# Performance work log

Measured on AMD Instinct MI355X. Metric: run time of the kernel, lower is better.

## Reference

```python
import jax, jax.numpy as jnp
import numpy as np

N = 100000
E = 1600000
IN_CH = 128
HID = 32
HEADS = 4
OUT_CH = 64
NEG_SLOPE = 0.2


def _gat_conv(x, src, dst, W, att_src, att_dst, bias, heads, out_ch):
    # PyG GATConv (concat=True, add_self_loops handled by caller via src/dst)
    n = x.shape[0]
    xp = (x @ W).reshape(n, heads, out_ch)                  # [N,H,C]
    a_src = (xp * att_src).sum(-1)                          # [N,H]
    a_dst = (xp * att_dst).sum(-1)                          # [N,H]
    e = jax.nn.leaky_relu(a_src[src] + a_dst[dst], NEG_SLOPE)  # [E,H]
    m = jax.ops.segment_max(e, dst, num_segments=n)         # per-dst max (safe: self-loops)
    ex = jnp.exp(e - m[dst])
    denom = jax.ops.segment_sum(ex, dst, num_segments=n)
    alpha = ex / denom[dst]                                  # [E,H]
    out = jax.ops.segment_sum(xp[src] * alpha[:, :, None], dst, num_segments=n)
    return out.reshape(n, heads * out_ch) + bias


def setup_inputs() -> dict:
    key = jax.random.key(0)
    ks = jax.random.split(key, 12)
    sc1 = 1.0 / np.sqrt(IN_CH)
    sc2 = 1.0 / np.sqrt(HID * HEADS * 2)
    return {
        "x_ppi": jax.random.normal(ks[0], (N, IN_CH), jnp.float32),
        "x_go": jax.random.normal(ks[1], (N, IN_CH), jnp.float32),
        "edge_index": jax.random.randint(ks[2], (2, E), 0, N, jnp.int32),
        "W1": jax.random.normal(ks[3], (IN_CH, HEADS * HID), jnp.float32) * sc1,
        "att_src1": jax.random.normal(ks[4], (HEADS, HID), jnp.float32) * sc1,
        "att_dst1": jax.random.normal(ks[5], (HEADS, HID), jnp.float32) * sc1,
        "b1": jnp.zeros((HEADS * HID,), jnp.float32),
        "W2": jax.random.normal(ks[6], (HID * HEADS * 2, OUT_CH), jnp.float32) * sc2,
        "att_src2": jax.random.normal(ks[7], (1, OUT_CH), jnp.float32) * sc2,
        "att_dst2": jax.random.normal(ks[8], (1, OUT_CH), jnp.float32) * sc2,
        "b2": jnp.zeros((OUT_CH,), jnp.float32),
    }


def reference(x_ppi, x_go, edge_index, W1, att_src1, att_dst1, b1, W2, att_src2, att_dst2, b2):
    loops = jnp.arange(N, dtype=edge_index.dtype)
    src = jnp.concatenate([edge_index[0], loops])
    dst = jnp.concatenate([edge_index[1], loops])
    h_ppi = _gat_conv(x_ppi, src, dst, W1, att_src1, att_dst1, b1, HEADS, HID)
    h_go = _gat_conv(x_go, src, dst, W1, att_src1, att_dst1, b1, HEADS, HID)
    h = jax.nn.relu(jnp.concatenate([h_ppi, h_go], axis=-1))  # [N, 2*H*HID]
    out = _gat_conv(h, src, dst, W2, att_src2, att_dst2, b2, 1, OUT_CH)
    return out
```

## Files before the change

kernel.cpp:

```cpp
#include <hip/hip_runtime.h>
#include <hip/hip_fp16.h>

constexpr int NN = 100000;
constexpr int EE = 1600000;
constexpr int ET = EE + NN;
constexpr int EQ = EE / 4;
constexpr int TQ = ET / 4;
constexpr int NBUK = (NN + 255) / 256;
constexpr int PB = 416;
constexpr float NEG = 0.2f;

typedef _Float16 f16x8 __attribute__((ext_vector_type(8)));
typedef _Float16 f16x4 __attribute__((ext_vector_type(4)));
typedef float    f32x4 __attribute__((ext_vector_type(4)));

__global__ __launch_bounds__(256) void k_bcount(const int4* __restrict__ dst4v,
                                                int* __restrict__ bucketCount) {
    __shared__ int bh[NBUK];
    for (int i = threadIdx.x; i < NBUK; i += 256) bh[i] = 0;
    __syncthreads();
    int gtid = blockIdx.x * 256 + threadIdx.x;
    for (int q = gtid; q < TQ; q += PB * 256) {
        int4 d;
        if (q < EQ) {
            d = dst4v[q];
        } else {
            int s0 = (q - EQ) * 4;
            d.x = s0; d.y = s0 + 1; d.z = s0 + 2; d.w = s0 + 3;
        }
        atomicAdd(&bh[d.x >> 8], 1);
        atomicAdd(&bh[d.y >> 8], 1);
        atomicAdd(&bh[d.z >> 8], 1);
        atomicAdd(&bh[d.w >> 8], 1);
    }
    __syncthreads();
    for (int i = threadIdx.x; i < NBUK; i += 256)
        if (bh[i]) atomicAdd(&bucketCount[i], bh[i]);
}

__global__ __launch_bounds__(512) void k_bscan(const int* __restrict__ bucketCount,
                                               int* __restrict__ bstart, int* __restrict__ gcur,
                                               int* __restrict__ rs) {
    __shared__ int sh[512];
    int t = threadIdx.x;
    int v = (t < NBUK) ? bucketCount[t] : 0;
    sh[t] = v;
    __syncthreads();
    for (int o = 1; o < 512; o <<= 1) {
        int u = (t >= o) ? sh[t - o] : 0;
        __syncthreads();
        sh[t] += u;
        __syncthreads();
    }
    if (t < NBUK) { bstart[t] = sh[t] - v; gcur[t] = sh[t] - v; }
    if (t == 0) { bstart[NBUK] = ET; rs[NN] = ET; }
}

__global__ __launch_bounds__(256) void k_bplace(const int4* __restrict__ src4v, const int4* __restrict__ dst4v,
                                                int* __restrict__ gcur, unsigned int* __restrict__ ebuf) {
    __shared__ int bh[NBUK];
    __shared__ int bbase[NBUK];
    for (int i = threadIdx.x; i < NBUK; i += 256) bh[i] = 0;
    __syncthreads();
    int gtid = blockIdx.x * 256 + threadIdx.x;

    int esrc[16];
    int emeta[16];
#pragma unroll
    for (int it = 0; it < 4; it++) {
        int q = gtid + it * (PB * 256);
        bool valid = q < TQ;
        int4 s, d;
        if (valid) {
            if (q < EQ) { s = src4v[q]; d = dst4v[q]; }
            else { int s0 = (q - EQ) * 4; s.x = s0; s.y = s0 + 1; s.z = s0 + 2; s.w = s0 + 3; d = s; }
        } else {
            s.x = s.y = s.z = s.w = 0; d = s;
        }
        int ss[4] = {s.x, s.y, s.z, s.w};
        int dd[4] = {d.x, d.y, d.z, d.w};
#pragma unroll
        for (int k = 0; k < 4; k++) {
            int idx = it * 4 + k;
            if (valid) {
                int b = dd[k] >> 8, l = dd[k] & 255;
                int r = atomicAdd(&bh[b], 1);
                esrc[idx]  = ss[k];
                emeta[idx] = (b << 21) | (l << 13) | r;
            } else {
                emeta[idx] = -1;
            }
        }
    }
    __syncthreads();
    for (int i = threadIdx.x; i < NBUK; i += 256)
        bbase[i] = bh[i] ? atomicAdd(&gcur[i], bh[i]) : 0;
    __syncthreads();
#pragma unroll
    for (int e = 0; e < 16; e++) {
        int me = emeta[e];
        if (me >= 0) {
            int b = me >> 21, l = (me >> 13) & 255, r = me & 8191;
            ebuf[bbase[b] + r] = ((unsigned)l << 24) | (unsigned)esrc[e];
        }
    }
}

__global__ __launch_bounds__(256) void k_csr(const unsigned int* __restrict__ ebuf,
                                             const int* __restrict__ bstart,
                                             int* __restrict__ rs, int* __restrict__ csr) {
    __shared__ int hist[256];
    __shared__ int sh[256];
    __shared__ int cur[256];
    int b = blockIdx.x;
    int t = threadIdx.x;
    int e0 = bstart[b], e1 = bstart[b + 1];
    hist[t] = 0;
    __syncthreads();
    for (int j = e0 + t; j < e1; j += 256)
        atomicAdd(&hist[ebuf[j] >> 24], 1);
    __syncthreads();
    int v = hist[t];
    sh[t] = v;
    __syncthreads();
    for (int o = 1; o < 256; o <<= 1) {
        int u = (t >= o) ? sh[t - o] : 0;
        __syncthreads();
        sh[t] += u;
        __syncthreads();
    }
    int excl = sh[t] - v;
    cur[t] = excl;
    int v0 = b * 256;
    if (v0 + t < NN) rs[v0 + t] = e0 + excl;
    __syncthreads();
    for (int j = e0 + t; j < e1; j += 256) {
        unsigned int e = ebuf[j];
        int l = (int)(e >> 24);
        int r = atomicAdd(&cur[l], 1);
        csr[e0 + r] = (int)(e & 0x00FFFFFFu);
    }
}

__global__ __launch_bounds__(256) void k_wprep(const float* __restrict__ W1, const float* __restrict__ W2,
                                               _Float16* __restrict__ w1T, _Float16* __restrict__ w2T) {
    int idx = blockIdx.x * 256 + threadIdx.x;
    if (idx < 128 * 128) {
        int nn = idx >> 7, k = idx & 127;
        w1T[idx] = (_Float16)W1[k * 128 + nn];
    }
    int i2 = idx - 128 * 128;
    if (i2 >= 0 && i2 < 64 * 256) {
        int nn = i2 >> 8, k = i2 & 255;
        w2T[i2] = (_Float16)W2[k * 64 + nn];
    }
}

template <int K, int C, bool SRCF32, int AMODE>
__global__ __launch_bounds__(256) void gemm_direct(const void* __restrict__ xv,
                                                   const _Float16* __restrict__ wT,
                                                   const float* __restrict__ as_w, const float* __restrict__ ad_w,
                                                   __half* __restrict__ xp,
                                                   float* __restrict__ att_s, float* __restrict__ att_d, int n) {
    constexpr int NT = C / 16;
    const int tid  = threadIdx.x;
    const int w    = tid >> 6;
    const int lane = tid & 63;
    const int quad = lane >> 4;
    const int l16  = lane & 15;
    const long r0  = (long)blockIdx.x * 128;
    const long row0 = r0 + w * 32 + l16;
    const long row1 = row0 + 16;

    f32x4 acc[2][NT];
#pragma unroll
    for (int s = 0; s < 2; s++)
#pragma unroll
        for (int t = 0; t < NT; t++) acc[s][t] = (f32x4){0.f, 0.f, 0.f, 0.f};

#pragma unroll
    for (int ks = 0; ks < K; ks += 32) {
        f16x8 a0 = (f16x8){0, 0, 0, 0, 0, 0, 0, 0};
        f16x8 a1 = (f16x8){0, 0, 0, 0, 0, 0, 0, 0};
        if (SRCF32) {
            if (row0 < n) {
                const float4* p = (const float4*)((const float*)xv + row0 * K + ks) + quad * 2;
                float4 u = p[0], v = p[1];
                a0 = (f16x8){(_Float16)u.x, (_Float16)u.y, (_Float16)u.z, (_Float16)u.w,
                             (_Float16)v.x, (_Float16)v.y, (_Float16)v.z, (_Float16)v.w};
            }
            if (row1 < n) {
                const float4* p = (const float4*)((const float*)xv + row1 * K + ks) + quad * 2;
                float4 u = p[0], v = p[1];
                a1 = (f16x8){(_Float16)u.x, (_Float16)u.y, (_Float16)u.z, (_Float16)u.w,
                             (_Float16)v.x, (_Float16)v.y, (_Float16)v.z, (_Float16)v.w};
            }
        } else {
            if (row0 < n) a0 = *(const f16x8*)((const _Float16*)xv + row0 * K + ks + quad * 8);
            if (row1 < n) a1 = *(const f16x8*)((const _Float16*)xv + row1 * K + ks + quad * 8);
        }
#pragma unroll
        for (int t = 0; t < NT; t++) {
            f16x8 b = *(const f16x8*)(wT + (long)(t * 16 + l16) * K + ks + quad * 8);
            acc[0][t] = __builtin_amdgcn_mfma_f32_16x16x32_f16(a0, b, acc[0][t], 0, 0, 0);
            acc[1][t] = __builtin_amdgcn_mfma_f32_16x16x32_f16(a1, b, acc[1][t], 0, 0, 0);
        }
    }

#pragma unroll
    for (int sub = 0; sub < 2; sub++) {
        long rb = r0 + w * 32 + sub * 16 + quad * 4;
#pragma unroll
        for (int t = 0; t < NT; t++) {
            int c = t * 16 + l16;
#pragma unroll
            for (int rg = 0; rg < 4; rg++) {
                long row = rb + rg;
                if (row < n) xp[row * (long)C + c] = __float2half(acc[sub][t][rg]);
            }
        }
    }

    if (AMODE == 1) {
        float asw[8], adw[8];
#pragma unroll
        for (int t = 0; t < 8; t++) {
            int ci = (t >> 1) * 32 + (t & 1) * 16 + l16;
            asw[t] = as_w[ci];
            adw[t] = ad_w[ci];
        }
#pragma unroll
        for (int sub = 0; sub < 2; sub++) {
#pragma unroll
            for (int rg = 0; rg < 4; rg++) {
                long row = r0 + w * 32 + sub * 16 + quad * 4 + rg;
                float hs[4] = {0.f, 0.f, 0.f, 0.f};
                float hd[4] = {0.f, 0.f, 0.f, 0.f};
#pragma unroll
                for (int t = 0; t < 8; t++) {
                    float av = acc[sub][t][rg];
                    hs[t >> 1] += av * asw[t];
                    hd[t >> 1] += av * adw[t];
                }
#pragma unroll
                for (int h = 0; h < 4; h++) {
                    hs[h] += __shfl_xor(hs[h], 1); hs[h] += __shfl_xor(hs[h], 2);
                    hs[h] += __shfl_xor(hs[h], 4); hs[h] += __shfl_xor(hs[h], 8);
                    hd[h] += __shfl_xor(hd[h], 1); hd[h] += __shfl_xor(hd[h], 2);
                    hd[h] += __shfl_xor(hd[h], 4); hd[h] += __shfl_xor(hd[h], 8);
                }
                if (l16 == 0 && row < n) {
                    ((float4*)att_s)[row] = make_float4(hs[0], hs[1], hs[2], hs[3]);
                    ((float4*)att_d)[row] = make_float4(hd[0], hd[1], hd[2], hd[3]);
                }
            }
        }
    }
    if (AMODE == 2) {
        float asw[NT], adw[NT];
#pragma unroll
        for (int t = 0; t < NT; t++) {
            asw[t] = as_w[t * 16 + l16];
            adw[t] = ad_w[t * 16 + l16];
        }
#pragma unroll
        for (int sub = 0; sub < 2; sub++) {
#pragma unroll
            for (int rg = 0; rg < 4; rg++) {
                long row = r0 + w * 32 + sub * 16 + quad * 4 + rg;
                float s = 0.f, d = 0.f;
#pragma unroll
                for (int t = 0; t < NT; t++) {
                    float av = acc[sub][t][rg];
                    s += av * asw[t];
                    d += av * adw[t];
                }
                s += __shfl_xor(s, 1); s += __shfl_xor(s, 2); s += __shfl_xor(s, 4); s += __shfl_xor(s, 8);
                d += __shfl_xor(d, 1); d += __shfl_xor(d, 2); d += __shfl_xor(d, 4); d += __shfl_xor(d, 8);
                if (l16 == 0 && row < n) {
                    att_s[row] = s;
                    att_d[row] = d;
                }
            }
        }
    }
}

__global__ __launch_bounds__(256) void conv1_pass(const int* __restrict__ rs, const int* __restrict__ csr,
                                                  const uint4* __restrict__ xp,
                                                  const float* __restrict__ att_s,
                                                  const float* __restrict__ att_d,
                                                  const float* __restrict__ bias,
                                                  __half* __restrict__ out, int off) {
    int v = blockIdx.x * 4 + (threadIdx.x >> 6);
    if (v >= NN) return;
    int lane = threadIdx.x & 63;
    int qw = lane >> 4;
    int m = lane & 15;
    int hd = m >> 2;
    int e0 = rs[v], e1 = rs[v + 1];

    float adv = att_d[v * 4 + hd];
    auto lrexp = [](float e) { e = (e > 0.f) ? e : NEG * e; return __expf(e); };

    float a[8];
#pragma unroll
    for (int i = 0; i < 8; i++) a[i] = 0.f;
    float d = 0.f;

    int j = e0;
    for (; j + 16 <= e1; j += 16) {
        int s[4]; float av[4]; uint4 r[4];
#pragma unroll
        for (int k = 0; k < 4; k++) s[k] = csr[j + 4 * k + qw];
#pragma unroll
        for (int k = 0; k < 4; k++) av[k] = att_s[s[k] * 4 + hd];
#pragma unroll
        for (int k = 0; k < 4; k++) r[k] = xp[(long)s[k] * 16 + m];
#pragma unroll
        for (int k = 0; k < 4; k++) {
            float w = lrexp(av[k] + adv);
            d += w;
            float2 f0 = __half22float2(*(__half2*)&r[k].x);
            float2 f1 = __half22float2(*(__half2*)&r[k].y);
            float2 f2 = __half22float2(*(__half2*)&r[k].z);
            float2 f3 = __half22float2(*(__half2*)&r[k].w);
            a[0] += w * f0.x; a[1] += w * f0.y;
            a[2] += w * f1.x; a[3] += w * f1.y;
            a[4] += w * f2.x; a[5] += w * f2.y;
            a[6] += w * f3.x; a[7] += w * f3.y;
        }
    }
    for (; j < e1; j += 4) {
        int jj = j + qw;
        int jc = (jj < e1) ? jj : (e1 - 1);
        int s = csr[jc];
        float av = att_s[s * 4 + hd];
        uint4 r = xp[(long)s * 16 + m];
        float w = (jj < e1) ? lrexp(av + adv) : 0.f;
        d += w;
        float2 f0 = __half22float2(*(__half2*)&r.x);
        float2 f1 = __half22float2(*(__half2*)&r.y);
        float2 f2 = __half22float2(*(__half2*)&r.z);
        float2 f3 = __half22float2(*(__half2*)&r.w);
        a[0] += w * f0.x; a[1] += w * f0.y;
        a[2] += w * f1.x; a[3] += w * f1.y;
        a[4] += w * f2.x; a[5] += w * f2.y;
        a[6] += w * f3.x; a[7] += w * f3.y;
    }

#pragma unroll
    for (int i = 0; i < 8; i++) {
        a[i] += __shfl_xor(a[i], 16);
        a[i] += __shfl_xor(a[i], 32);
    }
    d += __shfl_xor(d, 16);
    d += __shfl_xor(d, 32);

    if (qw == 0) {
        float inv = 1.0f / d;
        const float4* b4 = (const float4*)bias;
        float4 bA = b4[2 * m], bB = b4[2 * m + 1];
        __half2 o01 = __floats2half2_rn(fmaxf(a[0] * inv + bA.x, 0.f), fmaxf(a[1] * inv + bA.y, 0.f));
        __half2 o23 = __floats2half2_rn(fmaxf(a[2] * inv + bA.z, 0.f), fmaxf(a[3] * inv + bA.w, 0.f));
        __half2 o45 = __floats2half2_rn(fmaxf(a[4] * inv + bB.x, 0.f), fmaxf(a[5] * inv + bB.y, 0.f));
        __half2 o67 = __floats2half2_rn(fmaxf(a[6] * inv + bB.z, 0.f), fmaxf(a[7] * inv + bB.w, 0.f));
        uint4 st;
        st.x = *(unsigned int*)&o01;
        st.y = *(unsigned int*)&o23;
        st.z = *(unsigned int*)&o45;
        st.w = *(unsigned int*)&o67;
        *(uint4*)(out + (long)v * 256 + off + 8 * m) = st;
    }
}

__global__ __launch_bounds__(256) void conv2_edge(const int* __restrict__ rs, const int* __restrict__ csr,
                                                  const __half* __restrict__ xp,
                                                  const float* __restrict__ asrc,
                                                  const float* __restrict__ adst,
                                                  const float* __restrict__ bias,
                                                  float* __restrict__ out) {
    int v = blockIdx.x * 4 + (threadIdx.x >> 6);
    if (v >= NN) return;
    int lane = threadIdx.x & 63;
    int qw = lane >> 4;
    int m = lane & 15;
    int e0 = rs[v], e1 = rs[v + 1];
    const uint2* xp2 = (const uint2*)xp;

    float adv = adst[v];
    auto lrexp = [](float e) { e = (e > 0.f) ? e : NEG * e; return __expf(e); };

    float a0 = 0.f, a1 = 0.f, a2 = 0.f, a3 = 0.f, d = 0.f;

    int j = e0;
    for (; j + 16 <= e1; j += 16) {
        int s[4]; float av[4]; uint2 r[4];
#pragma unroll
        for (int k = 0; k < 4; k++) s[k] = csr[j + 4 * k + qw];
#pragma unroll
        for (int k = 0; k < 4; k++) av[k] = asrc[s[k]];
#pragma unroll
        for (int k = 0; k < 4; k++) r[k] = xp2[(long)s[k] * 16 + m];
#pragma unroll
        for (int k = 0; k < 4; k++) {
            float w = lrexp(av[k] + adv);
            d += w;
            float2 x01 = __half22float2(*(__half2*)&r[k].x);
            float2 x23 = __half22float2(*(__half2*)&r[k].y);
            a0 += w * x01.x; a1 += w * x01.y;
            a2 += w * x23.x; a3 += w * x23.y;
        }
    }
    for (; j < e1; j += 4) {
        int jj = j + qw;
        int jc = (jj < e1) ? jj : (e1 - 1);
        int s = csr[jc];
        float av = asrc[s];
        uint2 r = xp2[(long)s * 16 + m];
        float w = (jj < e1) ? lrexp(av + adv) : 0.f;
        d += w;
        float2 x01 = __half22float2(*(__half2*)&r.x);
        float2 x23 = __half22float2(*(__half2*)&r.y);
        a0 += w * x01.x; a1 += w * x01.y;
        a2 += w * x23.x; a3 += w * x23.y;
    }

    a0 += __shfl_xor(a0, 16); a1 += __shfl_xor(a1, 16);
    a2 += __shfl_xor(a2, 16); a3 += __shfl_xor(a3, 16);
    d  += __shfl_xor(d, 16);
    a0 += __shfl_xor(a0, 32); a1 += __shfl_xor(a1, 32);
    a2 += __shfl_xor(a2, 32); a3 += __shfl_xor(a3, 32);
    d  += __shfl_xor(d, 32);

    if (qw == 0) {
        float inv = 1.0f / d;
        float4 b4 = *(const float4*)&bias[4 * m];
        float4 o;
        o.x = a0 * inv + b4.x;
        o.y = a1 * inv + b4.y;
        o.z = a2 * inv + b4.z;
        o.w = a3 * inv + b4.w;
        *(float4*)&out[(long)v * 64 + 4 * m] = o;
    }
}

extern "C" void kernel_launch(void* const* d_in, const int* in_sizes, int n_in,
                              void* d_out, int out_size, void* d_ws, size_t ws_size,
                              hipStream_t stream) {
    const float* x_ppi = (const float*)d_in[0];
    const float* x_go  = (const float*)d_in[1];
    const int*   ei    = (const int*)d_in[2];
    const float* W1    = (const float*)d_in[3];
    const float* as1   = (const float*)d_in[4];
    const float* ad1   = (const float*)d_in[5];
    const float* b1    = (const float*)d_in[6];
    const float* W2    = (const float*)d_in[7];
    const float* as2   = (const float*)d_in[8];
    const float* ad2   = (const float*)d_in[9];
    const float* b2    = (const float*)d_in[10];
    float* out = (float*)d_out;

    char* ws = (char*)d_ws;
    size_t off = 0;
    auto alloc = [&](size_t bytes) -> void* {
        void* p = ws + off;
        off = (off + bytes + 255) & ~(size_t)255;
        return p;
    };
    int* bucketCount = (int*)alloc((size_t)NBUK * 4);
    int* bstart      = (int*)alloc((size_t)(NBUK + 1) * 4);
    int* gcur        = (int*)alloc((size_t)NBUK * 4);
    unsigned int* ebuf = (unsigned int*)alloc((size_t)ET * 4);
    int* rs      = (int*)alloc((size_t)(NN + 1) * 4);
    int* csr     = (int*)alloc((size_t)ET * 4);
    _Float16* w1T = (_Float16*)alloc((size_t)128 * 128 * 2);
    _Float16* w2T = (_Float16*)alloc((size_t)64 * 256 * 2);
    __half* xp_p = (__half*)alloc((size_t)NN * 128 * 2);
    __half* xp_g = (__half*)alloc((size_t)NN * 128 * 2);
    __half* xp2  = (__half*)alloc((size_t)NN * 64 * 2);
    float* attsp = (float*)alloc((size_t)NN * 4 * 4);
    float* attdp = (float*)alloc((size_t)NN * 4 * 4);
    float* attsg = (float*)alloc((size_t)NN * 4 * 4);
    float* attdg = (float*)alloc((size_t)NN * 4 * 4);
    float* asr2  = (float*)alloc((size_t)NN * 4);
    float* ads2  = (float*)alloc((size_t)NN * 4);
    __half* hbuf = (__half*)alloc((size_t)NN * 256 * 2);
    (void)ws_size; (void)in_sizes; (void)n_in; (void)out_size;

    const int GB = (NN + 127) / 128;

    hipMemsetAsync(bucketCount, 0, (size_t)NBUK * 4, stream);
    k_bcount<<<PB, 256, 0, stream>>>((const int4*)(ei + EE), bucketCount);
    k_bscan<<<1, 512, 0, stream>>>(bucketCount, bstart, gcur, rs);
    k_bplace<<<PB, 256, 0, stream>>>((const int4*)ei, (const int4*)(ei + EE), gcur, ebuf);
    k_csr<<<NBUK, 256, 0, stream>>>(ebuf, bstart, rs, csr);

    k_wprep<<<128, 256, 0, stream>>>(W1, W2, w1T, w2T);

    gemm_direct<128, 128, true, 1><<<GB, 256, 0, stream>>>(x_ppi, w1T, as1, ad1, xp_p, attsp, attdp, NN);
    gemm_direct<128, 128, true, 1><<<GB, 256, 0, stream>>>(x_go, w1T, as1, ad1, xp_g, attsg, attdg, NN);
    conv1_pass<<<NN / 4, 256, 0, stream>>>(rs, csr, (const uint4*)xp_p, attsp, attdp, b1, hbuf, 0);
    conv1_pass<<<NN / 4, 256, 0, stream>>>(rs, csr, (const uint4*)xp_g, attsg, attdg, b1, hbuf, 128);

    gemm_direct<256, 64, false, 2><<<GB, 256, 0, stream>>>(hbuf, w2T, as2, ad2, xp2, asr2, ads2, NN);
    conv2_edge<<<NN / 4, 256, 0, stream>>>(rs, csr, xp2, asr2, ads2, b2, out);
}
```

Measured before the change: 494.5 us.

## Interleave ppi/go projections and fuse both conv1 aggregations into one pass

```diff
diff --git a/kernel.cpp b/kernel.cpp
--- a/kernel.cpp
+++ b/kernel.cpp
@@ -8,142 +8,18 @@
 constexpr int TQ = ET / 4;
 constexpr int NBUK = (NN + 255) / 256;
 constexpr int PB = 416;
+constexpr int GB = (NN + 127) / 128;
 constexpr float NEG = 0.2f;
 
 typedef _Float16 f16x8 __attribute__((ext_vector_type(8)));
-typedef _Float16 f16x4 __attribute__((ext_vector_type(4)));
 typedef float    f32x4 __attribute__((ext_vector_type(4)));
 
-__global__ __launch_bounds__(256) void k_bcount(const int4* __restrict__ dst4v,
+__global__ __launch_bounds__(256) void k_wprep0(const float* __restrict__ W1, const float* __restrict__ W2,
+                                                _Float16* __restrict__ w1T, _Float16* __restrict__ w2T,
                                                 int* __restrict__ bucketCount) {
-    __shared__ int bh[NBUK];
-    for (int i = threadIdx.x; i < NBUK; i += 256) bh[i] = 0;
-    __syncthreads();
-    int gtid = blockIdx.x * 256 + threadIdx.x;
-    for (int q = gtid; q < TQ; q += PB * 256) {
-        int4 d;
-        if (q < EQ) {
-            d = dst4v[q];
-        } else {
-            int s0 = (q - EQ) * 4;
-            d.x = s0; d.y = s0 + 1; d.z = s0 + 2; d.w = s0 + 3;
-        }
-        atomicAdd(&bh[d.x >> 8], 1);
-        atomicAdd(&bh[d.y >> 8], 1);
-        atomicAdd(&bh[d.z >> 8], 1);
-        atomicAdd(&bh[d.w >> 8], 1);
-    }
-    __syncthreads();
-    for (int i = threadIdx.x; i < NBUK; i += 256)
-        if (bh[i]) atomicAdd(&bucketCount[i], bh[i]);
-}
-
-__global__ __launch_bounds__(512) void k_bscan(const int* __restrict__ bucketCount,
-                                               int* __restrict__ bstart, int* __restrict__ gcur,
-                                               int* __restrict__ rs) {
-    __shared__ int sh[512];
-    int t = threadIdx.x;
-    int v = (t < NBUK) ? bucketCount[t] : 0;
-    sh[t] = v;
-    __syncthreads();
-    for (int o = 1; o < 512; o <<= 1) {
-        int u = (t >= o) ? sh[t - o] : 0;
-        __syncthreads();
-        sh[t] += u;
-        __syncthreads();
-    }
-    if (t < NBUK) { bstart[t] = sh[t] - v; gcur[t] = sh[t] - v; }
-    if (t == 0) { bstart[NBUK] = ET; rs[NN] = ET; }
-}
-
-__global__ __launch_bounds__(256) void k_bplace(const int4* __restrict__ src4v, const int4* __restrict__ dst4v,
-                                                int* __restrict__ gcur, unsigned int* __restrict__ ebuf) {
-    __shared__ int bh[NBUK];
-    __shared__ int bbase[NBUK];
-    for (int i = threadIdx.x; i < NBUK; i += 256) bh[i] = 0;
-    __syncthreads();
-    int gtid = blockIdx.x * 256 + threadIdx.x;
-
-    int esrc[16];
-    int emeta[16];
-#pragma unroll
-    for (int it = 0; it < 4; it++) {
-        int q = gtid + it * (PB * 256);
-        bool valid = q < TQ;
-        int4 s, d;
-        if (valid) {
-            if (q < EQ) { s = src4v[q]; d = dst4v[q]; }
-            else { int s0 = (q - EQ) * 4; s.x = s0; s.y = s0 + 1; s.z = s0 + 2; s.w = s0 + 3; d = s; }
-        } else {
-            s.x = s.y = s.z = s.w = 0; d = s;
-        }
-        int ss[4] = {s.x, s.y, s.z, s.w};
-        int dd[4] = {d.x, d.y, d.z, d.w};
-#pragma unroll
-        for (int k = 0; k < 4; k++) {
-            int idx = it * 4 + k;
-            if (valid) {
-                int b = dd[k] >> 8, l = dd[k] & 255;
-                int r = atomicAdd(&bh[b], 1);
-                esrc[idx]  = ss[k];
-                emeta[idx] = (b << 21) | (l << 13) | r;
-            } else {
-                emeta[idx] = -1;
-            }
-        }
-    }
-    __syncthreads();
-    for (int i = threadIdx.x; i < NBUK; i += 256)
-        bbase[i] = bh[i] ? atomicAdd(&gcur[i], bh[i]) : 0;
-    __syncthreads();
-#pragma unroll
-    for (int e = 0; e < 16; e++) {
-        int me = emeta[e];
-        if (me >= 0) {
-            int b = me >> 21, l = (me >> 13) & 255, r = me & 8191;
-            ebuf[bbase[b] + r] = ((unsigned)l << 24) | (unsigned)esrc[e];
-        }
-    }
-}
-
-__global__ __launch_bounds__(256) void k_csr(const unsigned int* __restrict__ ebuf,
-                                             const int* __restrict__ bstart,
-                                             int* __restrict__ rs, int* __restrict__ csr) {
-    __shared__ int hist[256];
-    __shared__ int sh[256];
-    __shared__ int cur[256];
-    int b = blockIdx.x;
-    int t = threadIdx.x;
-    int e0 = bstart[b], e1 = bstart[b + 1];
-    hist[t] = 0;
-    __syncthreads();
-    for (int j = e0 + t; j < e1; j += 256)
-        atomicAdd(&hist[ebuf[j] >> 24], 1);
-    __syncthreads();
-    int v = hist[t];
-    sh[t] = v;
-    __syncthreads();
-    for (int o = 1; o < 256; o <<= 1) {
-        int u = (t >= o) ? sh[t - o] : 0;
-        __syncthreads();
-        sh[t] += u;
-        __syncthreads();
-    }
-    int excl = sh[t] - v;
-    cur[t] = excl;
-    int v0 = b * 256;
-    if (v0 + t < NN) rs[v0 + t] = e0 + excl;
-    __syncthreads();
-    for (int j = e0 + t; j < e1; j += 256) {
-        unsigned int e = ebuf[j];
-        int l = (int)(e >> 24);
-        int r = atomicAdd(&cur[l], 1);
-        csr[e0 + r] = (int)(e & 0x00FFFFFFu);
-    }
-}
-
-__global__ __launch_bounds__(256) void k_wprep(const float* __restrict__ W1, const float* __restrict__ W2,
-                                               _Float16* __restrict__ w1T, _Float16* __restrict__ w2T) {
+    if (blockIdx.x == 0) {
+        for (int i = threadIdx.x; i < NBUK; i += 256) bucketCount[i] = 0;
+    }
     int idx = blockIdx.x * 256 + threadIdx.x;
     if (idx < 128 * 128) {
         int nn = idx >> 7, k = idx & 127;
@@ -156,19 +32,19 @@
     }
 }
 
-template <int K, int C, bool SRCF32, int AMODE>
-__global__ __launch_bounds__(256) void gemm_direct(const void* __restrict__ xv,
-                                                   const _Float16* __restrict__ wT,
-                                                   const float* __restrict__ as_w, const float* __restrict__ ad_w,
-                                                   __half* __restrict__ xp,
-                                                   float* __restrict__ att_s, float* __restrict__ att_d, int n) {
+template <int K, int C, bool SRCF32, int AMODE, int OUTM, int SET>
+__device__ __forceinline__ void gemm_dev(int bx, const void* __restrict__ xv,
+                                         const _Float16* __restrict__ wT,
+                                         const float* __restrict__ as_w, const float* __restrict__ ad_w,
+                                         __half* __restrict__ xp,
+                                         float* __restrict__ att_s, float* __restrict__ att_d, int n) {
     constexpr int NT = C / 16;
     const int tid  = threadIdx.x;
     const int w    = tid >> 6;
     const int lane = tid & 63;
     const int quad = lane >> 4;
     const int l16  = lane & 15;
-    const long r0  = (long)blockIdx.x * 128;
+    const long r0  = (long)bx * 128;
     const long row0 = r0 + w * 32 + l16;
     const long row1 = row0 + 16;
 
@@ -216,7 +92,13 @@
 #pragma unroll
             for (int rg = 0; rg < 4; rg++) {
                 long row = rb + rg;
-                if (row < n) xp[row * (long)C + c] = __float2half(acc[sub][t][rg]);
+                if (row < n) {
+                    __half hv = __float2half(acc[sub][t][rg]);
+                    if (OUTM == 0)
+                        xp[row * 256 + ((c >> 1) << 2) + (c & 1) + SET * 2] = hv;
+                    else
+                        xp[row * (long)C + c] = hv;
+                }
             }
         }
     }
@@ -250,8 +132,11 @@
                     hd[h] += __shfl_xor(hd[h], 4); hd[h] += __shfl_xor(hd[h], 8);
                 }
                 if (l16 == 0 && row < n) {
-                    ((float4*)att_s)[row] = make_float4(hs[0], hs[1], hs[2], hs[3]);
-                    ((float4*)att_d)[row] = make_float4(hd[0], hd[1], hd[2], hd[3]);
+#pragma unroll
+                    for (int h = 0; h < 4; h++) {
+                        att_s[row * 8 + h * 2 + SET] = hs[h];
+                        att_d[row * 8 + h * 2 + SET] = hd[h];
+                    }
                 }
             }
         }
@@ -286,92 +171,240 @@
     }
 }
 
-__global__ __launch_bounds__(256) void conv1_pass(const int* __restrict__ rs, const int* __restrict__ csr,
-                                                  const uint4* __restrict__ xp,
-                                                  const float* __restrict__ att_s,
-                                                  const float* __restrict__ att_d,
-                                                  const float* __restrict__ bias,
-                                                  __half* __restrict__ out, int off) {
+__device__ __forceinline__ void bcount_dev(int bx, const int4* __restrict__ dst4v,
+                                           int* __restrict__ bucketCount) {
+    __shared__ int bh[NBUK];
+    for (int i = threadIdx.x; i < NBUK; i += 256) bh[i] = 0;
+    __syncthreads();
+    int gtid = bx * 256 + threadIdx.x;
+    for (int q = gtid; q < TQ; q += PB * 256) {
+        int4 d;
+        if (q < EQ) {
+            d = dst4v[q];
+        } else {
+            int s0 = (q - EQ) * 4;
+            d.x = s0; d.y = s0 + 1; d.z = s0 + 2; d.w = s0 + 3;
+        }
+        atomicAdd(&bh[d.x >> 8], 1);
+        atomicAdd(&bh[d.y >> 8], 1);
+        atomicAdd(&bh[d.z >> 8], 1);
+        atomicAdd(&bh[d.w >> 8], 1);
+    }
+    __syncthreads();
+    for (int i = threadIdx.x; i < NBUK; i += 256)
+        if (bh[i]) atomicAdd(&bucketCount[i], bh[i]);
+}
+
+__global__ __launch_bounds__(256) void megaA(const float* __restrict__ x_ppi, const float* __restrict__ x_go,
+                                             const int4* __restrict__ dst4v,
+                                             const _Float16* __restrict__ w1T,
+                                             const float* __restrict__ as1, const float* __restrict__ ad1,
+                                             __half* __restrict__ xpc,
+                                             float* __restrict__ att1s, float* __restrict__ att1d,
+                                             int* __restrict__ bucketCount) {
+    int bx = blockIdx.x;
+    if (bx < GB) {
+        gemm_dev<128, 128, true, 1, 0, 0>(bx, x_ppi, w1T, as1, ad1, xpc, att1s, att1d, NN);
+    } else if (bx < 2 * GB) {
+        gemm_dev<128, 128, true, 1, 0, 1>(bx - GB, x_go, w1T, as1, ad1, xpc, att1s, att1d, NN);
+    } else {
+        bcount_dev(bx - 2 * GB, dst4v, bucketCount);
+    }
+}
+
+__global__ __launch_bounds__(256) void gemm_k2(const __half* __restrict__ hbuf,
+                                               const _Float16* __restrict__ w2T,
+                                               const float* __restrict__ as2, const float* __restrict__ ad2,
+                                               __half* __restrict__ xp2,
+                                               float* __restrict__ asr2, float* __restrict__ ads2) {
+    gemm_dev<256, 64, false, 2, 1, 0>(blockIdx.x, hbuf, w2T, as2, ad2, xp2, asr2, ads2, NN);
+}
+
+__global__ __launch_bounds__(512) void k_bscan(const int* __restrict__ bucketCount,
+                                               int* __restrict__ bstart, int* __restrict__ gcur,
+                                               int* __restrict__ rs) {
+    __shared__ int sh[512];
+    int t = threadIdx.x;
+    int v = (t < NBUK) ? bucketCount[t] : 0;
+    sh[t] = v;
+    __syncthreads();
+    for (int o = 1; o < 512; o <<= 1) {
+        int u = (t >= o) ? sh[t - o] : 0;
+        __syncthreads();
+        sh[t] += u;
+        __syncthreads();
+    }
+    if (t < NBUK) { bstart[t] = sh[t] - v; gcur[t] = sh[t] - v; }
+    if (t == 0) { bstart[NBUK] = ET; rs[NN] = ET; }
+}
+
+__global__ __launch_bounds__(256) void k_bplace(const int4* __restrict__ src4v, const int4* __restrict__ dst4v,
+                                                int* __restrict__ gcur, unsigned int* __restrict__ ebuf) {
+    __shared__ int bh[NBUK];
+    __shared__ int bbase[NBUK];
+    for (int i = threadIdx.x; i < NBUK; i += 256) bh[i] = 0;
+    __syncthreads();
+    int gtid = blockIdx.x * 256 + threadIdx.x;
+
+    int esrc[16];
+    int emeta[16];
+#pragma unroll
+    for (int it = 0; it < 4; it++) {
+        int q = gtid + it * (PB * 256);
+        bool valid = q < TQ;
+        int4 s, d;
+        if (valid) {
+            if (q < EQ) { s = src4v[q]; d = dst4v[q]; }
+            else { int s0 = (q - EQ) * 4; s.x = s0; s.y = s0 + 1; s.z = s0 + 2; s.w = s0 + 3; d = s; }
+        } else {
+            s.x = s.y = s.z = s.w = 0; d = s;
+        }
+        int ss[4] = {s.x, s.y, s.z, s.w};
+        int dd[4] = {d.x, d.y, d.z, d.w};
+#pragma unroll
+        for (int k = 0; k < 4; k++) {
+            int idx = it * 4 + k;
+            if (valid) {
+                int b = dd[k] >> 8, l = dd[k] & 255;
+                int r = atomicAdd(&bh[b], 1);
+                esrc[idx]  = ss[k];
+                emeta[idx] = (b << 21) | (l << 13) | r;
+            } else {
+                emeta[idx] = -1;
+            }
+        }
+    }
+    __syncthreads();
+    for (int i = threadIdx.x; i < NBUK; i += 256)
+        bbase[i] = bh[i] ? atomicAdd(&gcur[i], bh[i]) : 0;
+    __syncthreads();
+#pragma unroll
+    for (int e = 0; e < 16; e++) {
+        int me = emeta[e];
+        if (me >= 0) {
+            int b = me >> 21, l = (me >> 13) & 255, r = me & 8191;
+            ebuf[bbase[b] + r] = ((unsigned)l << 24) | (unsigned)esrc[e];
+        }
+    }
+}
+
+__global__ __launch_bounds__(256) void k_csr(const unsigned int* __restrict__ ebuf,
+                                             const int* __restrict__ bstart,
+                                             int* __restrict__ rs, int* __restrict__ csr) {
+    __shared__ int hist[256];
+    __shared__ int sh[256];
+    __shared__ int cur[256];
+    int b = blockIdx.x;
+    int t = threadIdx.x;
+    int e0 = bstart[b], e1 = bstart[b + 1];
+    hist[t] = 0;
+    __syncthreads();
+    for (int j = e0 + t; j < e1; j += 256)
+        atomicAdd(&hist[ebuf[j] >> 24], 1);
+    __syncthreads();
+    int v = hist[t];
+    sh[t] = v;
+    __syncthreads();
+    for (int o = 1; o < 256; o <<= 1) {
+        int u = (t >= o) ? sh[t - o] : 0;
+        __syncthreads();
+        sh[t] += u;
+        __syncthreads();
+    }
+    int excl = sh[t] - v;
+    cur[t] = excl;
+    int v0 = b * 256;
+    if (v0 + t < NN) rs[v0 + t] = e0 + excl;
+    __syncthreads();
+    for (int j = e0 + t; j < e1; j += 256) {
+        unsigned int e = ebuf[j];
+        int l = (int)(e >> 24);
+        int r = atomicAdd(&cur[l], 1);
+        csr[e0 + r] = (int)(e & 0x00FFFFFFu);
+    }
+}
+
+__global__ __launch_bounds__(256) void conv1_packed(const int* __restrict__ rs, const int* __restrict__ csr,
+                                                    const uint4* __restrict__ xpc,
+                                                    const float2* __restrict__ att_s,
+                                                    const float2* __restrict__ att_d,
+                                                    const float* __restrict__ bias,
+                                                    __half* __restrict__ out) {
     int v = blockIdx.x * 4 + (threadIdx.x >> 6);
     if (v >= NN) return;
     int lane = threadIdx.x & 63;
-    int qw = lane >> 4;
-    int m = lane & 15;
-    int hd = m >> 2;
+    int h = lane >> 5;
+    int m = lane & 31;
+    int hd = m >> 3;
     int e0 = rs[v], e1 = rs[v + 1];
 
-    float adv = att_d[v * 4 + hd];
+    float2 ad = att_d[v * 4 + hd];
     auto lrexp = [](float e) { e = (e > 0.f) ? e : NEG * e; return __expf(e); };
 
-    float a[8];
-#pragma unroll
-    for (int i = 0; i < 8; i++) a[i] = 0.f;
-    float d = 0.f;
+    float ap0 = 0.f, ap1 = 0.f, ap2 = 0.f, ap3 = 0.f;
+    float ag0 = 0.f, ag1 = 0.f, ag2 = 0.f, ag3 = 0.f;
+    float dp = 0.f, dg = 0.f;
 
     int j = e0;
-    for (; j + 16 <= e1; j += 16) {
-        int s[4]; float av[4]; uint4 r[4];
-#pragma unroll
-        for (int k = 0; k < 4; k++) s[k] = csr[j + 4 * k + qw];
-#pragma unroll
-        for (int k = 0; k < 4; k++) av[k] = att_s[s[k] * 4 + hd];
-#pragma unroll
-        for (int k = 0; k < 4; k++) r[k] = xp[(long)s[k] * 16 + m];
-#pragma unroll
-        for (int k = 0; k < 4; k++) {
-            float w = lrexp(av[k] + adv);
-            d += w;
-            float2 f0 = __half22float2(*(__half2*)&r[k].x);
-            float2 f1 = __half22float2(*(__half2*)&r[k].y);
-            float2 f2 = __half22float2(*(__half2*)&r[k].z);
-            float2 f3 = __half22float2(*(__half2*)&r[k].w);
-            a[0] += w * f0.x; a[1] += w * f0.y;
-            a[2] += w * f1.x; a[3] += w * f1.y;
-            a[4] += w * f2.x; a[5] += w * f2.y;
-            a[6] += w * f3.x; a[7] += w * f3.y;
-        }
-    }
-    for (; j < e1; j += 4) {
-        int jj = j + qw;
+    for (; j + 8 <= e1; j += 8) {
+        int s[4]; float2 av[4]; uint4 r[4];
+#pragma unroll
+        for (int q = 0; q < 4; q++) s[q] = csr[j + 2 * q + h];
+#pragma unroll
+        for (int q = 0; q < 4; q++) av[q] = att_s[s[q] * 4 + hd];
+#pragma unroll
+        for (int q = 0; q < 4; q++) r[q] = xpc[(long)s[q] * 32 + m];
+#pragma unroll
+        for (int q = 0; q < 4; q++) {
+            float wx = lrexp(av[q].x + ad.x);
+            float wy = lrexp(av[q].y + ad.y);
+            dp += wx; dg += wy;
+            float2 p01 = __half22float2(*(__half2*)&r[q].x);
+            float2 g01 = __half22float2(*(__half2*)&r[q].y);
+            float2 p23 = __half22float2(*(__half2*)&r[q].z);
+            float2 g23 = __half22float2(*(__half2*)&r[q].w);
+            ap0 += wx * p01.x; ap1 += wx * p01.y; ap2 += wx * p23.x; ap3 += wx * p23.y;
+            ag0 += wy * g01.x; ag1 += wy * g01.y; ag2 += wy * g23.x; ag3 += wy * g23.y;
+        }
+    }
+    for (; j < e1; j += 2) {
+        int jj = j + h;
         int jc = (jj < e1) ? jj : (e1 - 1);
+        bool ok = jj < e1;
         int s = csr[jc];
-        float av = att_s[s * 4 + hd];
-        uint4 r = xp[(long)s * 16 + m];
-        float w = (jj < e1) ? lrexp(av + adv) : 0.f;
-        d += w;
-        float2 f0 = __half22float2(*(__half2*)&r.x);
-        float2 f1 = __half22float2(*(__half2*)&r.y);
-        float2 f2 = __half22float2(*(__half2*)&r.z);
-        float2 f3 = __half22float2(*(__half2*)&r.w);
-        a[0] += w * f0.x; a[1] += w * f0.y;
-        a[2] += w * f1.x; a[3] += w * f1.y;
-        a[4] += w * f2.x; a[5] += w * f2.y;
-        a[6] += w * f3.x; a[7] += w * f3.y;
-    }
-
-#pragma unroll
-    for (int i = 0; i < 8; i++) {
-        a[i] += __shfl_xor(a[i], 16);
-        a[i] += __shfl_xor(a[i], 32);
-    }
-    d += __shfl_xor(d, 16);
-    d += __shfl_xor(d, 32);
-
-    if (qw == 0) {
-        float inv = 1.0f / d;
-        const float4* b4 = (const float4*)bias;
-        float4 bA = b4[2 * m], bB = b4[2 * m + 1];
-        __half2 o01 = __floats2half2_rn(fmaxf(a[0] * inv + bA.x, 0.f), fmaxf(a[1] * inv + bA.y, 0.f));
-        __half2 o23 = __floats2half2_rn(fmaxf(a[2] * inv + bA.z, 0.f), fmaxf(a[3] * inv + bA.w, 0.f));
-        __half2 o45 = __floats2half2_rn(fmaxf(a[4] * inv + bB.x, 0.f), fmaxf(a[5] * inv + bB.y, 0.f));
-        __half2 o67 = __floats2half2_rn(fmaxf(a[6] * inv + bB.z, 0.f), fmaxf(a[7] * inv + bB.w, 0.f));
-        uint4 st;
-        st.x = *(unsigned int*)&o01;
-        st.y = *(unsigned int*)&o23;
-        st.z = *(unsigned int*)&o45;
-        st.w = *(unsigned int*)&o67;
-        *(uint4*)(out + (long)v * 256 + off + 8 * m) = st;
-    }
+        float2 av = att_s[s * 4 + hd];
+        uint4 r = xpc[(long)s * 32 + m];
+        float wx = ok ? lrexp(av.x + ad.x) : 0.f;
+        float wy = ok ? lrexp(av.y + ad.y) : 0.f;
+        dp += wx; dg += wy;
+        float2 p01 = __half22float2(*(__half2*)&r.x);
+        float2 g01 = __half22float2(*(__half2*)&r.y);
+        float2 p23 = __half22float2(*(__half2*)&r.z);
+        float2 g23 = __half22float2(*(__half2*)&r.w);
+        ap0 += wx * p01.x; ap1 += wx * p01.y; ap2 += wx * p23.x; ap3 += wx * p23.y;
+        ag0 += wy * g01.x; ag1 += wy * g01.y; ag2 += wy * g23.x; ag3 += wy * g23.y;
+    }
+
+    ap0 += __shfl_xor(ap0, 32); ap1 += __shfl_xor(ap1, 32);
+    ap2 += __shfl_xor(ap2, 32); ap3 += __shfl_xor(ap3, 32);
+    ag0 += __shfl_xor(ag0, 32); ag1 += __shfl_xor(ag1, 32);
+    ag2 += __shfl_xor(ag2, 32); ag3 += __shfl_xor(ag3, 32);
+    dp  += __shfl_xor(dp, 32);  dg  += __shfl_xor(dg, 32);
+
+    float ivp = 1.0f / dp, ivg = 1.0f / dg;
+    int c0 = 4 * m;
+    float4 b4 = *(const float4*)&bias[c0];
+    float inv = h ? ivg : ivp;
+    float a0 = h ? ag0 : ap0;
+    float a1 = h ? ag1 : ap1;
+    float a2 = h ? ag2 : ap2;
+    float a3 = h ? ag3 : ap3;
+    __half2 o01 = __floats2half2_rn(fmaxf(a0 * inv + b4.x, 0.f), fmaxf(a1 * inv + b4.y, 0.f));
+    __half2 o23 = __floats2half2_rn(fmaxf(a2 * inv + b4.z, 0.f), fmaxf(a3 * inv + b4.w, 0.f));
+    uint2 st;
+    st.x = *(unsigned int*)&o01;
+    st.y = *(unsigned int*)&o23;
+    *(uint2*)(out + (long)v * 256 + h * 128 + c0) = st;
 }
 
 __global__ __launch_bounds__(256) void conv2_edge(const int* __restrict__ rs, const int* __restrict__ csr,
@@ -476,33 +509,23 @@
     int* csr     = (int*)alloc((size_t)ET * 4);
     _Float16* w1T = (_Float16*)alloc((size_t)128 * 128 * 2);
     _Float16* w2T = (_Float16*)alloc((size_t)64 * 256 * 2);
-    __half* xp_p = (__half*)alloc((size_t)NN * 128 * 2);
-    __half* xp_g = (__half*)alloc((size_t)NN * 128 * 2);
+    __half* xpc  = (__half*)alloc((size_t)NN * 256 * 2);
     __half* xp2  = (__half*)alloc((size_t)NN * 64 * 2);
-    float* attsp = (float*)alloc((size_t)NN * 4 * 4);
-    float* attdp = (float*)alloc((size_t)NN * 4 * 4);
-    float* attsg = (float*)alloc((size_t)NN * 4 * 4);
-    float* attdg = (float*)alloc((size_t)NN * 4 * 4);
+    float* att1s = (float*)alloc((size_t)NN * 4 * 8);
+    float* att1d = (float*)alloc((size_t)NN * 4 * 8);
     float* asr2  = (float*)alloc((size_t)NN * 4);
     float* ads2  = (float*)alloc((size_t)NN * 4);
     __half* hbuf = (__half*)alloc((size_t)NN * 256 * 2);
     (void)ws_size; (void)in_sizes; (void)n_in; (void)out_size;
 
-    const int GB = (NN + 127) / 128;
-
-    hipMemsetAsync(bucketCount, 0, (size_t)NBUK * 4, stream);
-    k_bcount<<<PB, 256, 0, stream>>>((const int4*)(ei + EE), bucketCount);
+    k_wprep0<<<128, 256, 0, stream>>>(W1, W2, w1T, w2T, bucketCount);
+    megaA<<<2 * GB + PB, 256, 0, stream>>>(x_ppi, x_go, (const int4*)(ei + EE),
+                                           w1T, as1, ad1, xpc, att1s, att1d, bucketCount);
     k_bscan<<<1, 512, 0, stream>>>(bucketCount, bstart, gcur, rs);
     k_bplace<<<PB, 256, 0, stream>>>((const int4*)ei, (const int4*)(ei + EE), gcur, ebuf);
     k_csr<<<NBUK, 256, 0, stream>>>(ebuf, bstart, rs, csr);
-
-    k_wprep<<<128, 256, 0, stream>>>(W1, W2, w1T, w2T);
-
-    gemm_direct<128, 128, true, 1><<<GB, 256, 0, stream>>>(x_ppi, w1T, as1, ad1, xp_p, attsp, attdp, NN);
-    gemm_direct<128, 128, true, 1><<<GB, 256, 0, stream>>>(x_go, w1T, as1, ad1, xp_g, attsg, attdg, NN);
-    conv1_pass<<<NN / 4, 256, 0, stream>>>(rs, csr, (const uint4*)xp_p, attsp, attdp, b1, hbuf, 0);
-    conv1_pass<<<NN / 4, 256, 0, stream>>>(rs, csr, (const uint4*)xp_g, attsg, attdg, b1, hbuf, 128);
-
-    gemm_direct<256, 64, false, 2><<<GB, 256, 0, stream>>>(hbuf, w2T, as2, ad2, xp2, asr2, ads2, NN);
+    conv1_packed<<<NN / 4, 256, 0, stream>>>(rs, csr, (const uint4*)xpc,
+                                             (const float2*)att1s, (const float2*)att1d, b1, hbuf);
+    gemm_k2<<<GB, 256, 0, stream>>>(hbuf, w2T, as2, ad2, xp2, asr2, ads2);
     conv2_edge<<<NN / 4, 256, 0, stream>>>(rs, csr, xp2, asr2, ads2, b2, out);
 }
```

Measured after the change: 473.8 us. 4.2% less time.
